# Kernel optimization log

Measured on AMD Instinct MI355X. Metric: run time of the kernel, lower is better.

## Reference

```python
import jax, jax.numpy as jnp
import numpy as np

B, N, F, U = 4, 4096, 256, 128
NEG = -1.0e9


def setup_inputs() -> dict:
    key = jax.random.key(0)
    k1, k2, k3, k4, k5 = jax.random.split(key, 5)
    inputs = jax.random.normal(k1, (B, N, F), dtype=jnp.float32)
    # Glorot-normal-like scales
    w = jax.random.normal(k2, (F, U), dtype=jnp.float32) * np.sqrt(2.0 / (F + U)).astype(np.float32)
    ai = jax.random.normal(k3, (U, N), dtype=jnp.float32) * np.sqrt(2.0 / (U + N)).astype(np.float32)
    aj = jax.random.normal(k4, (U, N), dtype=jnp.float32) * np.sqrt(2.0 / (U + N)).astype(np.float32)
    a = (jax.random.uniform(k5, (N, N)) < 0.004).astype(jnp.float32)
    adj = jnp.maximum(a, a.T)
    return {"inputs": inputs, "w": w, "ai": ai, "aj": aj, "adj": adj}


def reference(inputs, w, ai, aj, adj):
    # f: [B, N, U]
    f = jnp.einsum('bnf,fu->bnu', inputs, w)
    # self_attn[b,i,j] = (f ai)[b,i,j]; other_attn = transpose([0,2,1]) of (f aj)
    self_attn = jnp.einsum('bnu,um->bnm', f, ai)          # [B, N, N]
    other_attn = jnp.einsum('bnu,um->bmn', f, aj)         # transposed [B, N, N]
    mask = adj + jnp.eye(N, dtype=adj.dtype)              # allow self + neighbors
    attn = self_attn + other_attn + NEG * (1.0 - mask)
    attn = jax.nn.softmax(attn, axis=1)                   # softmax over rows (axis=1)
    # out[b,j,u] = sum_i f[b,i,u] * attn[b,i,j]
    out = jnp.einsum('biu,bij->bju', f, attn)
    return jax.nn.relu(out), attn
```

## Files before the change

kernel.cpp:

```cpp
#include <hip/hip_runtime.h>
#include <hip/hip_bf16.h>

#define NN 4096
#define UU 128
#define BB 4
#define FF 256
#define MAXD 128
#define ZB 1024

typedef float fv4 __attribute__((ext_vector_type(4)));

__device__ __forceinline__ unsigned short f2bf(float x) {
    unsigned int u = __float_as_uint(x);
    unsigned int r = (u + 0x7fffu + ((u >> 16) & 1u)) >> 16;
    return (unsigned short)r;
}
__device__ __forceinline__ float bf2f(unsigned short h) {
    return __uint_as_float(((unsigned int)h) << 16);
}

template <int CTRL, int RMASK>
__device__ __forceinline__ float dpp_step(float x) {
    int ti = __builtin_amdgcn_update_dpp(0, __float_as_int(x), CTRL, RMASK, 0xf, true);
    return x + __int_as_float(ti);
}
__device__ __forceinline__ float wave_sum_dpp(float x) {
    x = dpp_step<0x111, 0xf>(x);
    x = dpp_step<0x112, 0xf>(x);
    x = dpp_step<0x114, 0xf>(x);
    x = dpp_step<0x118, 0xf>(x);
    x = dpp_step<0x142, 0xa>(x);
    x = dpp_step<0x143, 0xc>(x);
    return __int_as_float(__builtin_amdgcn_readlane(__float_as_int(x), 63));
}

__global__ __launch_bounds__(256) void stage1(const float* __restrict__ A,
                                              const float* __restrict__ Wm,
                                              const float* __restrict__ adj,
                                              const float* __restrict__ ai,
                                              const float* __restrict__ aj,
                                              unsigned short* __restrict__ F,
                                              unsigned short* __restrict__ csc,
                                              int* __restrict__ cnt,
                                              int* __restrict__ dblf,
                                              unsigned short* __restrict__ aiT,
                                              unsigned short* __restrict__ ajT) {
    __shared__ __align__(16) char smem[43008];
    int t = threadIdx.x;
    int bid = blockIdx.x;

    if (bid < 512) {
        float (*As)[36]  = (float(*)[36])smem;
        float (*Ws)[132] = (float(*)[132])(smem + 9216);
        int r0 = bid * 32;
        int cg = t & 31;
        int rg = t >> 5;
        float acc[4][4] = {};
        for (int kc = 0; kc < FF; kc += 64) {
            {
                int row = t >> 3;
                int kb = (t & 7) * 8;
                const float* ap = A + (size_t)(r0 + row) * FF + kc + kb;
                float4 v0 = *(const float4*)(ap);
                float4 v1 = *(const float4*)(ap + 4);
                As[kb + 0][row] = v0.x; As[kb + 1][row] = v0.y;
                As[kb + 2][row] = v0.z; As[kb + 3][row] = v0.w;
                As[kb + 4][row] = v1.x; As[kb + 5][row] = v1.y;
                As[kb + 6][row] = v1.z; As[kb + 7][row] = v1.w;
            }
#pragma unroll
            for (int q = 0; q < 8; q++) {
                int idx = q * 256 + t;
                int k = idx >> 5;
                int c4 = (idx & 31) * 4;
                *(float4*)&Ws[k][c4] = *(const float4*)(Wm + (size_t)(kc + k) * UU + c4);
            }
            __syncthreads();
#pragma unroll 8
            for (int kk = 0; kk < 64; kk++) {
                float4 a4 = *(const float4*)&As[kk][rg * 4];
                float4 w4 = *(const float4*)&Ws[kk][cg * 4];
                acc[0][0] += a4.x * w4.x; acc[0][1] += a4.x * w4.y; acc[0][2] += a4.x * w4.z; acc[0][3] += a4.x * w4.w;
                acc[1][0] += a4.y * w4.x; acc[1][1] += a4.y * w4.y; acc[1][2] += a4.y * w4.z; acc[1][3] += a4.y * w4.w;
                acc[2][0] += a4.z * w4.x; acc[2][1] += a4.z * w4.y; acc[2][2] += a4.z * w4.z; acc[2][3] += a4.z * w4.w;
                acc[3][0] += a4.w * w4.x; acc[3][1] += a4.w * w4.y; acc[3][2] += a4.w * w4.z; acc[3][3] += a4.w * w4.w;
            }
            __syncthreads();
        }
#pragma unroll
        for (int i = 0; i < 4; i++) {
            ushort4 h;
            h.x = f2bf(acc[i][0]); h.y = f2bf(acc[i][1]);
            h.z = f2bf(acc[i][2]); h.w = f2bf(acc[i][3]);
            *(ushort4*)(F + (size_t)(r0 + rg * 4 + i) * UU + cg * 4) = h;
        }
    } else if (bid < 4608) {
        unsigned short* tmp = (unsigned short*)smem;
        int* cd = (int*)(smem + 256);
        int j = bid - 512;
        if (t == 0) { cd[0] = 0; cd[1] = 0; }
        __syncthreads();
        const float4* row = (const float4*)(adj + (size_t)j * NN);
#pragma unroll
        for (int k = 0; k < 4; k++) {
            int q = t + k * 256;
            float4 v = row[q];
            int base = q * 4;
            float vals[4] = {v.x, v.y, v.z, v.w};
#pragma unroll
            for (int s = 0; s < 4; s++) {
                int i = base + s;
                bool nz = (vals[s] != 0.0f);
                if (i == j) { if (nz) cd[1] = 1; nz = true; }
                if (nz) {
                    int p = atomicAdd(&cd[0], 1);
                    if (p < MAXD) tmp[p] = (unsigned short)i;
                }
            }
        }
        __syncthreads();
        int M = cd[0] < MAXD ? cd[0] : MAXD;
        if (t < M) csc[(size_t)j * MAXD + t] = tmp[t];
        if (t == 0) { cnt[j] = M; dblf[j] = cd[1]; }
    } else {
        float (*tile)[33] = (float(*)[33])smem;
        int r = bid - 4608;
        int z = r >> 9;
        int rem = r & 511;
        int n0 = (rem >> 2) * 32;
        int u0 = (rem & 3) * 32;
        const float* src = z ? aj : ai;
        unsigned short* dst = z ? ajT : aiT;
        int tx = t & 31;
        int ty = t >> 5;
        for (int rr = 0; rr < 32; rr += 8)
            tile[ty + rr][tx] = src[(size_t)(u0 + ty + rr) * NN + n0 + tx];
        __syncthreads();
        for (int rr = 0; rr < 32; rr += 8)
            dst[(size_t)(n0 + ty + rr) * UU + u0 + tx] = f2bf(tile[tx][ty + rr]);
    }
}

__global__ __launch_bounds__(256) void gat_zc(const unsigned short* __restrict__ csc,
                                              const int* __restrict__ cnt,
                                              const int* __restrict__ dblf,
                                              const unsigned short* __restrict__ f,
                                              const unsigned short* __restrict__ aiT,
                                              const unsigned short* __restrict__ ajT,
                                              float* __restrict__ out,
                                              float* __restrict__ tmpex,
                                              float* __restrict__ attn) {
    int tid = threadIdx.x;
    if (blockIdx.x >= NN) {
        size_t base = (size_t)(blockIdx.x - NN) * ((size_t)BB * NN * NN / ZB);
        fv4* p = (fv4*)(attn + base) + tid;
        fv4 z = {0.f, 0.f, 0.f, 0.f};
#pragma unroll 8
        for (int q = 0; q < 64; q++)
            __builtin_nontemporal_store(z, p + q * 256);
        return;
    }

    __shared__ unsigned short sidx[MAXD];
    int j = blockIdx.x;
    int lane = tid & 63, b = tid >> 6;
    int M = cnt[j];
    int oneh = dblf[j];
    if (tid < MAXD) sidx[tid] = csc[(size_t)j * MAXD + tid];

    const unsigned short* fb = f + (size_t)b * NN * UU;
    float* te = tmpex + ((size_t)b * NN + j) * MAXD;
    ushort2 fjh = *(const ushort2*)(fb + (size_t)j * UU + 2 * lane);
    float fjx = bf2f(fjh.x), fjy = bf2f(fjh.y);

    if (oneh) {
        int g0 = csc[(size_t)j * MAXD + lane];
        int g1 = csc[(size_t)j * MAXD + lane + 64];
        if (lane < M)      te[lane]      = (g0 == j) ? 1.0f : 0.0f;
        if (lane + 64 < M) te[lane + 64] = (g1 == j) ? 1.0f : 0.0f;
        float2 o;
        o.x = fjx > 0.0f ? fjx : 0.0f;
        o.y = fjy > 0.0f ? fjy : 0.0f;
        *(float2*)(out + ((size_t)(b * NN + j)) * UU + 2 * lane) = o;
        return;
    }
    __syncthreads();

    ushort2 aih = *(const ushort2*)(aiT + (size_t)j * UU + 2 * lane);
    float aix = bf2f(aih.x), aiy = bf2f(aih.y);
    float denom = 0.0f, acc0 = 0.0f, acc1 = 0.0f;
    float keep0 = 0.0f, keep1 = 0.0f;

    int e = 0;
    for (; e + 2 <= M; e += 2) {
        int ia = sidx[e], ib2 = sidx[e + 1];
        ushort2 fha = *(const ushort2*)(fb + (size_t)ia * UU + 2 * lane);
        ushort2 aha = *(const ushort2*)(ajT + (size_t)ia * UU + 2 * lane);
        ushort2 fhb = *(const ushort2*)(fb + (size_t)ib2 * UU + 2 * lane);
        ushort2 ahb = *(const ushort2*)(ajT + (size_t)ib2 * UU + 2 * lane);
        float fax = bf2f(fha.x), fay = bf2f(fha.y);
        float fbx = bf2f(fhb.x), fby = bf2f(fhb.y);
        float pa = fax * aix + fay * aiy + fjx * bf2f(aha.x) + fjy * bf2f(aha.y);
        float pb = fbx * aix + fby * aiy + fjx * bf2f(ahb.x) + fjy * bf2f(ahb.y);
        float sa = wave_sum_dpp(pa);
        float sb = wave_sum_dpp(pb);
        float exa = __expf(sa);
        float exb = __expf(sb);
        denom += exa + exb;
        acc0 += exa * fax + exb * fbx;
        acc1 += exa * fay + exb * fby;
        if ((e & 63) == lane)       { if (e < 64)     keep0 = exa; else keep1 = exa; }
        if (((e + 1) & 63) == lane) { if (e + 1 < 64) keep0 = exb; else keep1 = exb; }
    }
    for (; e < M; e++) {
        int i = sidx[e];
        ushort2 fih = *(const ushort2*)(fb + (size_t)i * UU + 2 * lane);
        ushort2 ajh = *(const ushort2*)(ajT + (size_t)i * UU + 2 * lane);
        float fix = bf2f(fih.x), fiy = bf2f(fih.y);
        float p = fix * aix + fiy * aiy + fjx * bf2f(ajh.x) + fjy * bf2f(ajh.y);
        float ex = __expf(wave_sum_dpp(p));
        denom += ex;
        acc0 += ex * fix;
        acc1 += ex * fiy;
        if ((e & 63) == lane) { if (e < 64) keep0 = ex; else keep1 = ex; }
    }
    float inv = 1.0f / denom;

    float2 o;
    o.x = acc0 * inv; o.y = acc1 * inv;
    o.x = o.x > 0.0f ? o.x : 0.0f;
    o.y = o.y > 0.0f ? o.y : 0.0f;
    *(float2*)(out + ((size_t)(b * NN + j)) * UU + 2 * lane) = o;

    if (lane < M)      te[lane]      = keep0 * inv;
    if (lane + 64 < M) te[lane + 64] = keep1 * inv;
}

__global__ __launch_bounds__(256) void attn_scatter(const unsigned short* __restrict__ csc,
                                                    const int* __restrict__ cnt,
                                                    const float* __restrict__ tmpex,
                                                    float* __restrict__ attn) {
    int j = blockIdx.x, tid = threadIdx.x;
    int lane = tid & 63, b = tid >> 6;
    int M = cnt[j];
    const float* te = tmpex + ((size_t)b * NN + j) * MAXD;
    if (lane < M) {
        int i = csc[(size_t)j * MAXD + lane];
        __builtin_nontemporal_store(te[lane], &attn[((size_t)(b * NN + i)) * NN + j]);
    }
    if (lane + 64 < M) {
        int i = csc[(size_t)j * MAXD + lane + 64];
        __builtin_nontemporal_store(te[lane + 64], &attn[((size_t)(b * NN + i)) * NN + j]);
    }
}

extern "C" void kernel_launch(void* const* d_in, const int* in_sizes, int n_in,
                              void* d_out, int out_size, void* d_ws, size_t ws_size,
                              hipStream_t stream) {
    const float* inputs = (const float*)d_in[0];
    const float* w      = (const float*)d_in[1];
    const float* ai     = (const float*)d_in[2];
    const float* aj     = (const float*)d_in[3];
    const float* adj    = (const float*)d_in[4];

    float* out  = (float*)d_out;
    float* attn = out + (size_t)BB * NN * UU;

    unsigned short* f   = (unsigned short*)d_ws;
    unsigned short* aiT = f + (size_t)BB * NN * UU;
    unsigned short* ajT = aiT + (size_t)NN * UU;
    unsigned short* csc = ajT + (size_t)NN * UU;
    int* cnt  = (int*)(csc + (size_t)NN * MAXD);
    int* dblf = cnt + NN;
    float* tmpex = (float*)(dblf + NN);

    stage1<<<5632, 256, 0, stream>>>(inputs, w, adj, ai, aj, f, csc, cnt, dblf, aiT, ajT);
    gat_zc<<<NN + ZB, 256, 0, stream>>>(csc, cnt, dblf, f, aiT, ajT, out, tmpex, attn);
    attn_scatter<<<NN, 256, 0, stream>>>(csc, cnt, tmpex, attn);
}
```

Baseline: 409.1 us.

## Move attn zero-fill into stage1 and scatter attention directly from gat kernel

```diff
diff --git a/kernel.cpp b/kernel.cpp
--- a/kernel.cpp
+++ b/kernel.cpp
@@ -6,7 +6,7 @@
 #define BB 4
 #define FF 256
 #define MAXD 128
-#define ZB 1024
+#define ZBLK 2048
 
 typedef float fv4 __attribute__((ext_vector_type(4)));
 
@@ -44,15 +44,28 @@
                                               int* __restrict__ cnt,
                                               int* __restrict__ dblf,
                                               unsigned short* __restrict__ aiT,
-                                              unsigned short* __restrict__ ajT) {
+                                              unsigned short* __restrict__ ajT,
+                                              float* __restrict__ attn) {
     __shared__ __align__(16) char smem[43008];
     int t = threadIdx.x;
     int bid = blockIdx.x;
 
-    if (bid < 512) {
+    int m15 = bid % 15;
+    if (m15 < 4) {
+        int zidx = (bid / 15) * 4 + m15;
+        fv4 z = {0.f, 0.f, 0.f, 0.f};
+        fv4* p = (fv4*)attn + (size_t)zidx * 8192 + t;
+#pragma unroll 8
+        for (int q = 0; q < 32; q++)
+            p[q * 256] = z;
+        return;
+    }
+    int r = (bid / 15) * 11 + (m15 - 4);
+
+    if (r < 512) {
         float (*As)[36]  = (float(*)[36])smem;
         float (*Ws)[132] = (float(*)[132])(smem + 9216);
-        int r0 = bid * 32;
+        int r0 = r * 32;
         int cg = t & 31;
         int rg = t >> 5;
         float acc[4][4] = {};
@@ -94,10 +107,10 @@
             h.z = f2bf(acc[i][2]); h.w = f2bf(acc[i][3]);
             *(ushort4*)(F + (size_t)(r0 + rg * 4 + i) * UU + cg * 4) = h;
         }
-    } else if (bid < 4608) {
+    } else if (r < 4608) {
         unsigned short* tmp = (unsigned short*)smem;
         int* cd = (int*)(smem + 256);
-        int j = bid - 512;
+        int j = r - 512;
         if (t == 0) { cd[0] = 0; cd[1] = 0; }
         __syncthreads();
         const float4* row = (const float4*)(adj + (size_t)j * NN);
@@ -124,9 +137,9 @@
         if (t == 0) { cnt[j] = M; dblf[j] = cd[1]; }
     } else {
         float (*tile)[33] = (float(*)[33])smem;
-        int r = bid - 4608;
-        int z = r >> 9;
-        int rem = r & 511;
+        int rr2 = r - 4608;
+        int z = rr2 >> 9;
+        int rem = rr2 & 511;
         int n0 = (rem >> 2) * 32;
         int u0 = (rem & 3) * 32;
         const float* src = z ? aj : ai;
@@ -148,20 +161,9 @@
                                               const unsigned short* __restrict__ aiT,
                                               const unsigned short* __restrict__ ajT,
                                               float* __restrict__ out,
-                                              float* __restrict__ tmpex,
                                               float* __restrict__ attn) {
+    __shared__ unsigned short sidx[MAXD];
     int tid = threadIdx.x;
-    if (blockIdx.x >= NN) {
-        size_t base = (size_t)(blockIdx.x - NN) * ((size_t)BB * NN * NN / ZB);
-        fv4* p = (fv4*)(attn + base) + tid;
-        fv4 z = {0.f, 0.f, 0.f, 0.f};
-#pragma unroll 8
-        for (int q = 0; q < 64; q++)
-            __builtin_nontemporal_store(z, p + q * 256);
-        return;
-    }
-
-    __shared__ unsigned short sidx[MAXD];
     int j = blockIdx.x;
     int lane = tid & 63, b = tid >> 6;
     int M = cnt[j];
@@ -169,15 +171,12 @@
     if (tid < MAXD) sidx[tid] = csc[(size_t)j * MAXD + tid];
 
     const unsigned short* fb = f + (size_t)b * NN * UU;
-    float* te = tmpex + ((size_t)b * NN + j) * MAXD;
     ushort2 fjh = *(const ushort2*)(fb + (size_t)j * UU + 2 * lane);
     float fjx = bf2f(fjh.x), fjy = bf2f(fjh.y);
 
     if (oneh) {
-        int g0 = csc[(size_t)j * MAXD + lane];
-        int g1 = csc[(size_t)j * MAXD + lane + 64];
-        if (lane < M)      te[lane]      = (g0 == j) ? 1.0f : 0.0f;
-        if (lane + 64 < M) te[lane + 64] = (g1 == j) ? 1.0f : 0.0f;
+        if (lane == 0)
+            attn[((size_t)(b * NN + j)) * NN + j] = 1.0f;
         float2 o;
         o.x = fjx > 0.0f ? fjx : 0.0f;
         o.y = fjy > 0.0f ? fjy : 0.0f;
@@ -232,25 +231,13 @@
     o.y = o.y > 0.0f ? o.y : 0.0f;
     *(float2*)(out + ((size_t)(b * NN + j)) * UU + 2 * lane) = o;
 
-    if (lane < M)      te[lane]      = keep0 * inv;
-    if (lane + 64 < M) te[lane + 64] = keep1 * inv;
-}
-
-__global__ __launch_bounds__(256) void attn_scatter(const unsigned short* __restrict__ csc,
-                                                    const int* __restrict__ cnt,
-                                                    const float* __restrict__ tmpex,
-                                                    float* __restrict__ attn) {
-    int j = blockIdx.x, tid = threadIdx.x;
-    int lane = tid & 63, b = tid >> 6;
-    int M = cnt[j];
-    const float* te = tmpex + ((size_t)b * NN + j) * MAXD;
     if (lane < M) {
-        int i = csc[(size_t)j * MAXD + lane];
-        __builtin_nontemporal_store(te[lane], &attn[((size_t)(b * NN + i)) * NN + j]);
+        int i0 = sidx[lane];
+        __builtin_nontemporal_store(keep0 * inv, &attn[((size_t)(b * NN + i0)) * NN + j]);
     }
     if (lane + 64 < M) {
-        int i = csc[(size_t)j * MAXD + lane + 64];
-        __builtin_nontemporal_store(te[lane + 64], &attn[((size_t)(b * NN + i)) * NN + j]);
+        int i1 = sidx[lane + 64];
+        __builtin_nontemporal_store(keep1 * inv, &attn[((size_t)(b * NN + i1)) * NN + j]);
     }
 }
 
@@ -272,9 +259,7 @@
     unsigned short* csc = ajT + (size_t)NN * UU;
     int* cnt  = (int*)(csc + (size_t)NN * MAXD);
     int* dblf = cnt + NN;
-    float* tmpex = (float*)(dblf + NN);
-
-    stage1<<<5632, 256, 0, stream>>>(inputs, w, adj, ai, aj, f, csc, cnt, dblf, aiT, ajT);
-    gat_zc<<<NN + ZB, 256, 0, stream>>>(csc, cnt, dblf, f, aiT, ajT, out, tmpex, attn);
-    attn_scatter<<<NN, 256, 0, stream>>>(csc, cnt, tmpex, attn);
-}
+
+    stage1<<<7680, 256, 0, stream>>>(inputs, w, adj, ai, aj, f, csc, cnt, dblf, aiT, ajT, attn);
+    gat_zc<<<NN, 256, 0, stream>>>(csc, cnt, dblf, f, aiT, ajT, out, attn);
+}
```

Measured after the change: 395.0 us. -3.4%, faster.

## Write attention rows densely from shared memory instead of zero-fill plus scatter

Applied to the files above, without the earlier changes.

```diff
diff --git a/kernel.cpp b/kernel.cpp
--- a/kernel.cpp
+++ b/kernel.cpp
@@ -6,7 +6,6 @@
 #define BB 4
 #define FF 256
 #define MAXD 128
-#define ZB 1024
 
 typedef float fv4 __attribute__((ext_vector_type(4)));
 
@@ -45,31 +44,28 @@
                                               int* __restrict__ dblf,
                                               unsigned short* __restrict__ aiT,
                                               unsigned short* __restrict__ ajT) {
-    __shared__ __align__(16) char smem[43008];
+    __shared__ __align__(16) char smem[21504];
     int t = threadIdx.x;
     int bid = blockIdx.x;
 
     if (bid < 512) {
         float (*As)[36]  = (float(*)[36])smem;
-        float (*Ws)[132] = (float(*)[132])(smem + 9216);
+        float (*Ws)[132] = (float(*)[132])(smem + 4608);
         int r0 = bid * 32;
         int cg = t & 31;
         int rg = t >> 5;
         float acc[4][4] = {};
-        for (int kc = 0; kc < FF; kc += 64) {
+        for (int kc = 0; kc < FF; kc += 32) {
             {
                 int row = t >> 3;
-                int kb = (t & 7) * 8;
+                int kb = (t & 7) * 4;
                 const float* ap = A + (size_t)(r0 + row) * FF + kc + kb;
                 float4 v0 = *(const float4*)(ap);
-                float4 v1 = *(const float4*)(ap + 4);
                 As[kb + 0][row] = v0.x; As[kb + 1][row] = v0.y;
                 As[kb + 2][row] = v0.z; As[kb + 3][row] = v0.w;
-                As[kb + 4][row] = v1.x; As[kb + 5][row] = v1.y;
-                As[kb + 6][row] = v1.z; As[kb + 7][row] = v1.w;
-            }
-#pragma unroll
-            for (int q = 0; q < 8; q++) {
+            }
+#pragma unroll
+            for (int q = 0; q < 4; q++) {
                 int idx = q * 256 + t;
                 int k = idx >> 5;
                 int c4 = (idx & 31) * 4;
@@ -77,7 +73,7 @@
             }
             __syncthreads();
 #pragma unroll 8
-            for (int kk = 0; kk < 64; kk++) {
+            for (int kk = 0; kk < 32; kk++) {
                 float4 a4 = *(const float4*)&As[kk][rg * 4];
                 float4 w4 = *(const float4*)&Ws[kk][cg * 4];
                 acc[0][0] += a4.x * w4.x; acc[0][1] += a4.x * w4.y; acc[0][2] += a4.x * w4.z; acc[0][3] += a4.x * w4.w;
@@ -141,27 +137,16 @@
     }
 }
 
-__global__ __launch_bounds__(256) void gat_zc(const unsigned short* __restrict__ csc,
-                                              const int* __restrict__ cnt,
-                                              const int* __restrict__ dblf,
-                                              const unsigned short* __restrict__ f,
-                                              const unsigned short* __restrict__ aiT,
-                                              const unsigned short* __restrict__ ajT,
-                                              float* __restrict__ out,
-                                              float* __restrict__ tmpex,
-                                              float* __restrict__ attn) {
+__global__ __launch_bounds__(256) void gat_cols(const unsigned short* __restrict__ csc,
+                                                const int* __restrict__ cnt,
+                                                const int* __restrict__ dblf,
+                                                const unsigned short* __restrict__ f,
+                                                const unsigned short* __restrict__ aiT,
+                                                const unsigned short* __restrict__ ajT,
+                                                float* __restrict__ out,
+                                                float* __restrict__ invden) {
+    __shared__ unsigned short sidx[MAXD];
     int tid = threadIdx.x;
-    if (blockIdx.x >= NN) {
-        size_t base = (size_t)(blockIdx.x - NN) * ((size_t)BB * NN * NN / ZB);
-        fv4* p = (fv4*)(attn + base) + tid;
-        fv4 z = {0.f, 0.f, 0.f, 0.f};
-#pragma unroll 8
-        for (int q = 0; q < 64; q++)
-            __builtin_nontemporal_store(z, p + q * 256);
-        return;
-    }
-
-    __shared__ unsigned short sidx[MAXD];
     int j = blockIdx.x;
     int lane = tid & 63, b = tid >> 6;
     int M = cnt[j];
@@ -169,15 +154,10 @@
     if (tid < MAXD) sidx[tid] = csc[(size_t)j * MAXD + tid];
 
     const unsigned short* fb = f + (size_t)b * NN * UU;
-    float* te = tmpex + ((size_t)b * NN + j) * MAXD;
     ushort2 fjh = *(const ushort2*)(fb + (size_t)j * UU + 2 * lane);
     float fjx = bf2f(fjh.x), fjy = bf2f(fjh.y);
 
     if (oneh) {
-        int g0 = csc[(size_t)j * MAXD + lane];
-        int g1 = csc[(size_t)j * MAXD + lane + 64];
-        if (lane < M)      te[lane]      = (g0 == j) ? 1.0f : 0.0f;
-        if (lane + 64 < M) te[lane + 64] = (g1 == j) ? 1.0f : 0.0f;
         float2 o;
         o.x = fjx > 0.0f ? fjx : 0.0f;
         o.y = fjy > 0.0f ? fjy : 0.0f;
@@ -189,7 +169,6 @@
     ushort2 aih = *(const ushort2*)(aiT + (size_t)j * UU + 2 * lane);
     float aix = bf2f(aih.x), aiy = bf2f(aih.y);
     float denom = 0.0f, acc0 = 0.0f, acc1 = 0.0f;
-    float keep0 = 0.0f, keep1 = 0.0f;
 
     int e = 0;
     for (; e + 2 <= M; e += 2) {
@@ -209,8 +188,6 @@
         denom += exa + exb;
         acc0 += exa * fax + exb * fbx;
         acc1 += exa * fay + exb * fby;
-        if ((e & 63) == lane)       { if (e < 64)     keep0 = exa; else keep1 = exa; }
-        if (((e + 1) & 63) == lane) { if (e + 1 < 64) keep0 = exb; else keep1 = exb; }
     }
     for (; e < M; e++) {
         int i = sidx[e];
@@ -222,7 +199,6 @@
         denom += ex;
         acc0 += ex * fix;
         acc1 += ex * fiy;
-        if ((e & 63) == lane) { if (e < 64) keep0 = ex; else keep1 = ex; }
     }
     float inv = 1.0f / denom;
 
@@ -232,25 +208,62 @@
     o.y = o.y > 0.0f ? o.y : 0.0f;
     *(float2*)(out + ((size_t)(b * NN + j)) * UU + 2 * lane) = o;
 
-    if (lane < M)      te[lane]      = keep0 * inv;
-    if (lane + 64 < M) te[lane + 64] = keep1 * inv;
-}
-
-__global__ __launch_bounds__(256) void attn_scatter(const unsigned short* __restrict__ csc,
-                                                    const int* __restrict__ cnt,
-                                                    const float* __restrict__ tmpex,
-                                                    float* __restrict__ attn) {
-    int j = blockIdx.x, tid = threadIdx.x;
-    int lane = tid & 63, b = tid >> 6;
-    int M = cnt[j];
-    const float* te = tmpex + ((size_t)b * NN + j) * MAXD;
-    if (lane < M) {
-        int i = csc[(size_t)j * MAXD + lane];
-        __builtin_nontemporal_store(te[lane], &attn[((size_t)(b * NN + i)) * NN + j]);
-    }
-    if (lane + 64 < M) {
-        int i = csc[(size_t)j * MAXD + lane + 64];
-        __builtin_nontemporal_store(te[lane + 64], &attn[((size_t)(b * NN + i)) * NN + j]);
+    if (lane == 0) invden[(size_t)b * NN + j] = inv;
+}
+
+__global__ __launch_bounds__(256) void gat_rows(const unsigned short* __restrict__ csc,
+                                                const int* __restrict__ cnt,
+                                                const int* __restrict__ dblf,
+                                                const unsigned short* __restrict__ f,
+                                                const unsigned short* __restrict__ aiT,
+                                                const unsigned short* __restrict__ ajT,
+                                                const float* __restrict__ invden,
+                                                float* __restrict__ attn) {
+    __shared__ float rowv[NN];
+    __shared__ unsigned short sidx[MAXD];
+    int tid = threadIdx.x;
+    int bi = blockIdx.x;
+    int b = bi >> 12;
+    int i = bi & (NN - 1);
+
+    float4 z4 = {0.f, 0.f, 0.f, 0.f};
+#pragma unroll
+    for (int q = 0; q < 4; q++)
+        *(float4*)&rowv[(q * 256 + tid) * 4] = z4;
+    int M = cnt[i];
+    if (tid < MAXD) sidx[tid] = csc[(size_t)i * MAXD + tid];
+    __syncthreads();
+
+    int lane = tid & 63, w = tid >> 6;
+    const unsigned short* fb = f + (size_t)b * NN * UU;
+    ushort2 fih = *(const ushort2*)(fb + (size_t)i * UU + 2 * lane);
+    float fix_ = bf2f(fih.x), fiy_ = bf2f(fih.y);
+    ushort2 ajh = *(const ushort2*)(ajT + (size_t)i * UU + 2 * lane);
+    float ajx = bf2f(ajh.x), ajy = bf2f(ajh.y);
+
+    for (int e = w; e < M; e += 4) {
+        int j = sidx[e];
+        float val;
+        if (dblf[j]) {
+            val = (i == j) ? 1.0f : 0.0f;
+        } else {
+            ushort2 fjh = *(const ushort2*)(fb + (size_t)j * UU + 2 * lane);
+            ushort2 aih = *(const ushort2*)(aiT + (size_t)j * UU + 2 * lane);
+            float p = fix_ * bf2f(aih.x) + fiy_ * bf2f(aih.y)
+                    + bf2f(fjh.x) * ajx + bf2f(fjh.y) * ajy;
+            float s = wave_sum_dpp(p);
+            val = __expf(s) * invden[(size_t)b * NN + j];
+        }
+        if (lane == 0) rowv[j] = val;
+    }
+    __syncthreads();
+
+    float* dst = attn + (size_t)bi * NN;
+#pragma unroll
+    for (int q = 0; q < 4; q++) {
+        int c = (q * 256 + tid) * 4;
+        fv4 v = *(fv4*)&rowv[c];
+        __builtin_nontemporal_store(v, (fv4*)(dst + c));
     }
 }
 
@@ -272,9 +285,9 @@
     unsigned short* csc = ajT + (size_t)NN * UU;
     int* cnt  = (int*)(csc + (size_t)NN * MAXD);
     int* dblf = cnt + NN;
-    float* tmpex = (float*)(dblf + NN);
+    float* invden = (float*)(dblf + NN);
 
     stage1<<<5632, 256, 0, stream>>>(inputs, w, adj, ai, aj, f, csc, cnt, dblf, aiT, ajT);
-    gat_zc<<<NN + ZB, 256, 0, stream>>>(csc, cnt, dblf, f, aiT, ajT, out, tmpex, attn);
-    attn_scatter<<<NN, 256, 0, stream>>>(csc, cnt, tmpex, attn);
-}
+    gat_cols<<<NN, 256, 0, stream>>>(csc, cnt, dblf, f, aiT, ajT, out, invden);
+    gat_rows<<<BB * NN, 256, 0, stream>>>(csc, cnt, dblf, f, aiT, ajT, invden, attn);
+}
```

New measurement: 387.7 us. 1.06x faster.
